# Performance work log

Hardware: AMD Instinct MI355X
Metric: run time of the kernel (lower is better)

## Reference

```python
import jax, jax.numpy as jnp
import numpy as np

N, CH = 65536, 256
B, K, CTX = 8, 256, 768
H, D = 8, 64
NPB = N // B  # points per batch (scene)


def setup_inputs() -> dict:
    key = jax.random.key(0)
    ks = jax.random.split(key, 8)
    xF = jax.random.normal(ks[0], (N, CH), dtype=jnp.float32)
    context = jax.random.normal(ks[1], (B, K, CTX), dtype=jnp.float32)
    # decomposition_permutations: a random partition of the N sparse points into B groups
    perm = jax.random.permutation(ks[2], N).reshape(B, NPB).astype(jnp.int32)
    Wq = jax.random.normal(ks[3], (CH, H * D), dtype=jnp.float32) * 0.02
    Wk = jax.random.normal(ks[4], (CTX, H * D), dtype=jnp.float32) * 0.02
    Wv = jax.random.normal(ks[5], (CTX, H * D), dtype=jnp.float32) * 0.02
    Wout = jax.random.normal(ks[6], (H * D, CH), dtype=jnp.float32) * 0.02
    b_out = jnp.zeros((CH,), dtype=jnp.float32)
    return {"xF": xF, "context": context, "perm": perm,
            "Wq": Wq, "Wk": Wk, "Wv": Wv, "Wout": Wout, "b_out": b_out}


def reference(xF, context, perm, Wq, Wk, Wv, Wout, b_out):
    scale = D ** -0.5
    q = (xF @ Wq).reshape(N, H, D)                     # to_q (1x1 conv == linear)
    k = (context @ Wk).reshape(B, K, H, D)             # to_k
    v = (context @ Wv).reshape(B, K, H, D)             # to_v
    qg = q[perm]                                        # gather: [B, NPB, H, D]
    attn = jax.nn.softmax(scale * jnp.einsum('bqhd,bkhd->bhqk', qg, k), axis=-1)
    o = jnp.einsum('bhqk,bkhd->bqhd', attn, v).reshape(B * NPB, H * D)
    # inverse-permutation scatter back to sparse-tensor order: ft[inv_perm]
    ft = jnp.zeros((N, H * D), o.dtype).at[perm.reshape(-1)].set(o)
    out = ft @ Wout + b_out                             # to_out
    return out + xF                                     # residual
```

## Files before the change

kernel.cpp:

```cpp
#include <hip/hip_runtime.h>

typedef unsigned short u16;
typedef __attribute__((ext_vector_type(8))) short bf16x8;
typedef __attribute__((ext_vector_type(4))) float f32x4;
typedef __attribute__((ext_vector_type(4))) int i32x4;
typedef __attribute__((ext_vector_type(2))) int i32x2;

#define N_PTS   65536
#define CH_DIM  256
#define BATCH   8
#define KTOK    256
#define CTX_DIM 768
#define NHEAD   8
#define HD      64
#define HDIM    512
#define NPB     8192

__device__ __forceinline__ u16 f2bf(float f) {
    union { float f; unsigned u; } v; v.f = f;
    unsigned r = v.u + 0x7fffu + ((v.u >> 16) & 1u);
    return (u16)(r >> 16);
}
__device__ __forceinline__ unsigned cvtpk(float lo, float hi) {
    unsigned r;
    asm("v_cvt_pk_bf16_f32 %0, %1, %2" : "=v"(r) : "v"(lo), "v"(hi));
    return r;
}
__device__ __forceinline__ float exp2_hw(float x) {
    float r;
    asm("v_exp_f32 %0, %1" : "=v"(r) : "v"(x));
    return r;
}
__device__ __forceinline__ float max3f(float a, float b, float c) {
    float r;
    asm("v_max3_f32 %0, %1, %2, %3" : "=v"(r) : "v"(a), "v"(b), "v"(c));
    return r;
}

__device__ __forceinline__ void gll16(const void* g, void* l) {
    __builtin_amdgcn_global_load_lds(
        (const __attribute__((address_space(1))) void*)g,
        (__attribute__((address_space(3))) void*)l, 16, 0, 0);
}

__global__ void convk(const float* __restrict__ src, u16* __restrict__ dst, int n8) {
    int i = blockIdx.x * blockDim.x + threadIdx.x;
    int st = gridDim.x * blockDim.x;
    for (; i < n8; i += st) {
        const float* p = src + (size_t)i * 8;
        f32x4 a = *(const f32x4*)p;
        f32x4 b = *(const f32x4*)(p + 4);
        i32x4 o;
        o[0] = (int)cvtpk(a[0], a[1]);
        o[1] = (int)cvtpk(a[2], a[3]);
        o[2] = (int)cvtpk(b[0], b[1]);
        o[3] = (int)cvtpk(b[2], b[3]);
        *(i32x4*)&dst[(size_t)i * 8] = o;
    }
}

__global__ void tconvk(const float* __restrict__ W, u16* __restrict__ WT, int R, int C) {
    int i = blockIdx.x * blockDim.x + threadIdx.x;
    if (i >= R * C) return;
    WT[i] = f2bf(W[(size_t)(i % R) * C + i / R]);
}

__global__ void tconv3k(const float* __restrict__ Wq, const float* __restrict__ Wk,
                        const float* __restrict__ Wv,
                        u16* __restrict__ WqT, u16* __restrict__ WkvT) {
    int i = blockIdx.x * blockDim.x + threadIdx.x;
    if (i < 131072) {
        WqT[i] = f2bf(Wq[(size_t)(i % 256) * 512 + i / 256]);
    } else if (i < 524288) {
        int j = i - 131072;
        WkvT[j] = f2bf(Wk[(size_t)(j % 768) * 512 + j / 768]);
    } else if (i < 917504) {
        int j = i - 524288;
        WkvT[393216 + j] = f2bf(Wv[(size_t)(j % 768) * 512 + j / 768]);
    }
}

template <int KC, bool OUT_F32>
__global__ __launch_bounds__(256, 3) void gemm_bt(
    const u16* __restrict__ A, const u16* __restrict__ BT, void* __restrict__ Cv,
    int M, int N,
    const float* __restrict__ bias, const float* __restrict__ resid, float oscale)
{
    __shared__ __align__(16) u16 As[2][128 * 32];
    __shared__ __align__(16) u16 Bs[2][128 * 32];

    const int tid  = threadIdx.x;
    const int lane = tid & 63;
    const int w    = tid >> 6;
    const int wm   = w & 1;
    const int wn   = w >> 1;

    const int nwg = gridDim.x * gridDim.y;
    const int wg  = blockIdx.y * gridDim.x + blockIdx.x;
    const int swz = (wg & 7) * (nwg >> 3) + (wg >> 3);
    const int n0  = (swz % gridDim.x) * 128;
    const int m0  = (swz / gridDim.x) * 128;

    const int l15  = lane & 15;
    const int quad = lane >> 4;

    f32x4 acc[4][4];
#pragma unroll
    for (int i = 0; i < 4; i++)
#pragma unroll
        for (int j = 0; j < 4; j++) { acc[i][j][0]=0.f; acc[i][j][1]=0.f; acc[i][j][2]=0.f; acc[i][j][3]=0.f; }

    const int sr = tid >> 2;
    const int sc = (tid & 3) * 8;
    const u16* Abase = A  + (size_t)(m0 + sr) * KC + sc;
    const u16* Bbase = BT + (size_t)(n0 + sr) * KC + sc;
    const size_t rowStep = (size_t)64 * KC;
    const int d8 = tid * 8;

    gll16(Abase,           &As[0][d8]);
    gll16(Abase + rowStep, &As[0][d8 + 2048]);
    gll16(Bbase,           &Bs[0][d8]);
    gll16(Bbase + rowStep, &Bs[0][d8 + 2048]);
    asm volatile("s_waitcnt vmcnt(0)" ::: "memory");
    __builtin_amdgcn_s_barrier();
    __builtin_amdgcn_sched_barrier(0);

    constexpr int ntile = KC >> 5;
    int cur = 0;
    for (int t = 0; t < ntile; ++t) {
        if (t + 1 < ntile) {
            const u16* An = Abase + ((t + 1) << 5);
            const u16* Bn = Bbase + ((t + 1) << 5);
            const int nxt = cur ^ 1;
            gll16(An,           &As[nxt][d8]);
            gll16(An + rowStep, &As[nxt][d8 + 2048]);
            gll16(Bn,           &Bs[nxt][d8]);
            gll16(Bn + rowStep, &Bs[nxt][d8 + 2048]);
        }
        bf16x8 af[4], bfr[4];
#pragma unroll
        for (int rt = 0; rt < 4; rt++)
            af[rt] = *(const bf16x8*)&As[cur][(wm * 64 + rt * 16 + l15) * 32 + quad * 8];
#pragma unroll
        for (int nt = 0; nt < 4; nt++)
            bfr[nt] = *(const bf16x8*)&Bs[cur][(wn * 64 + nt * 16 + l15) * 32 + quad * 8];
#pragma unroll
        for (int rt = 0; rt < 4; rt++)
#pragma unroll
            for (int nt = 0; nt < 4; nt++)
                acc[rt][nt] = __builtin_amdgcn_mfma_f32_16x16x32_bf16(bfr[nt], af[rt], acc[rt][nt], 0, 0, 0);
        asm volatile("s_waitcnt vmcnt(0)" ::: "memory");
        __builtin_amdgcn_sched_barrier(0);
        __builtin_amdgcn_s_barrier();
        __builtin_amdgcn_sched_barrier(0);
        cur ^= 1;
    }

    if (OUT_F32) {
#pragma unroll
        for (int rt = 0; rt < 4; rt++) {
            int m = m0 + wm * 64 + rt * 16 + l15;
#pragma unroll
            for (int nt = 0; nt < 4; nt++) {
                int nb = n0 + wn * 64 + nt * 16 + quad * 4;
                f32x4 v  = acc[rt][nt];
                f32x4 bv = *(const f32x4*)&bias[nb];
                f32x4 rv = *(const f32x4*)&resid[(size_t)m * N + nb];
#pragma unroll
                for (int r = 0; r < 4; r++) v[r] += bv[r] + rv[r];
                *(f32x4*)&((float*)Cv)[(size_t)m * N + nb] = v;
            }
        }
    } else {
#pragma unroll
        for (int rt = 0; rt < 4; rt++) {
            int m = m0 + wm * 64 + rt * 16 + l15;
#pragma unroll
            for (int nt = 0; nt < 4; nt++) {
                int nb = n0 + wn * 64 + nt * 16 + quad * 4;
                union { unsigned u[2]; i32x2 q; } pk;
                pk.u[0] = cvtpk(acc[rt][nt][0] * oscale, acc[rt][nt][1] * oscale);
                pk.u[1] = cvtpk(acc[rt][nt][2] * oscale, acc[rt][nt][3] * oscale);
                *(i32x2*)&((u16*)Cv)[(size_t)m * N + nb] = pk.q;
            }
        }
    }
}

__global__ __launch_bounds__(256, 4) void gemm_kv(
    const u16* __restrict__ A, const u16* __restrict__ BT,
    u16* __restrict__ kd, u16* __restrict__ vtd)
{
    __shared__ __align__(16) u16 As[2][64 * 32];
    __shared__ __align__(16) u16 Bs[2][64 * 32];
    const int K = CTX_DIM;

    const int tid  = threadIdx.x;
    const int lane = tid & 63;
    const int w    = tid >> 6;
    const int wm   = w & 1;
    const int wn   = w >> 1;

    const int nwg = gridDim.x * gridDim.y;
    const int wg  = blockIdx.y * gridDim.x + blockIdx.x;
    const int swz = (wg & 7) * (nwg >> 3) + (wg >> 3);
    const int n0  = (swz % gridDim.x) * 64;
    const int m0  = (swz / gridDim.x) * 64;

    const int l15  = lane & 15;
    const int quad = lane >> 4;

    f32x4 acc[2][2];
#pragma unroll
    for (int i = 0; i < 2; i++)
#pragma unroll
        for (int j = 0; j < 2; j++) { acc[i][j][0]=0.f; acc[i][j][1]=0.f; acc[i][j][2]=0.f; acc[i][j][3]=0.f; }

    const int sr = tid >> 2;
    const int sc = (tid & 3) * 8;
    const u16* Abase = A  + (size_t)(m0 + sr) * K + sc;
    const u16* Bbase = BT + (size_t)(n0 + sr) * K + sc;
    const int d8 = tid * 8;

    gll16(Abase, &As[0][d8]);
    gll16(Bbase, &Bs[0][d8]);
    asm volatile("s_waitcnt vmcnt(0)" ::: "memory");
    __builtin_amdgcn_s_barrier();
    __builtin_amdgcn_sched_barrier(0);

    const int ntile = K >> 5;
    int cur = 0;
    for (int t = 0; t < ntile; ++t) {
        if (t + 1 < ntile) {
            const int nxt = cur ^ 1;
            gll16(Abase + ((t + 1) << 5), &As[nxt][d8]);
            gll16(Bbase + ((t + 1) << 5), &Bs[nxt][d8]);
        }
        bf16x8 af[2], bfr[2];
#pragma unroll
        for (int rt = 0; rt < 2; rt++)
            af[rt] = *(const bf16x8*)&As[cur][(wm * 32 + rt * 16 + l15) * 32 + quad * 8];
#pragma unroll
        for (int nt = 0; nt < 2; nt++)
            bfr[nt] = *(const bf16x8*)&Bs[cur][(wn * 32 + nt * 16 + l15) * 32 + quad * 8];
#pragma unroll
        for (int rt = 0; rt < 2; rt++)
#pragma unroll
            for (int nt = 0; nt < 2; nt++)
                acc[rt][nt] = __builtin_amdgcn_mfma_f32_16x16x32_bf16(af[rt], bfr[nt], acc[rt][nt], 0, 0, 0);
        asm volatile("s_waitcnt vmcnt(0)" ::: "memory");
        __builtin_amdgcn_sched_barrier(0);
        __builtin_amdgcn_s_barrier();
        __builtin_amdgcn_sched_barrier(0);
        cur ^= 1;
    }

    if (n0 < 512) {
#pragma unroll
        for (int nt = 0; nt < 2; nt++) {
            int col = n0 + wn * 32 + nt * 16 + l15;
#pragma unroll
            for (int rt = 0; rt < 2; rt++) {
#pragma unroll
                for (int r = 0; r < 4; r++) {
                    int row = m0 + wm * 32 + rt * 16 + quad * 4 + r;
                    kd[(size_t)row * HDIM + col] = f2bf(acc[rt][nt][r]);
                }
            }
        }
    } else {
#pragma unroll
        for (int nt = 0; nt < 2; nt++) {
            int col = (n0 - 512) + wn * 32 + nt * 16 + l15;
            int hh = col >> 6, dd = col & 63;
#pragma unroll
            for (int rt = 0; rt < 2; rt++) {
                int row = m0 + wm * 32 + rt * 16 + quad * 4;
                int bb = row >> 8, jb = row & 255;
                int jp = (jb & 0xE0) | ((jb & 0x0C) << 1) | ((jb & 0x10) >> 2);
                union { unsigned u[2]; i32x2 q; } pk;
                pk.u[0] = cvtpk(acc[rt][nt][0], acc[rt][nt][1]);
                pk.u[1] = cvtpk(acc[rt][nt][2], acc[rt][nt][3]);
                *(i32x2*)&vtd[(((size_t)(bb * 8 + hh)) * 64 + dd) * 256 + jp] = pk.q;
            }
        }
    }
}

#define KS2 72
#define VS2 264
__global__ __launch_bounds__(256, 4) void attn_mfma(
    const u16* qbuf, const u16* __restrict__ kbuf,
    const u16* __restrict__ vbufT, const int* __restrict__ perm,
    u16* ft)
{
    __shared__ __align__(16) u16 smem[18432];
    u16* Ks = smem;
    u16* Vt = smem;

    const int tid   = threadIdx.x;
    const int lane  = tid & 63;
    const int w     = tid >> 6;
    const int chunk = blockIdx.x;
    const int bh    = blockIdx.y;
    const int b     = bh >> 3;
    const int h     = bh & 7;
    const int l15   = lane & 15;
    const int quad  = lane >> 4;

    const int prow = perm[b * NPB + chunk * 64 + w * 16 + l15];
    const u16* qrow = qbuf + (size_t)prow * HDIM + h * HD;
    bf16x8 qf0 = *(const bf16x8*)&qrow[quad * 8];
    bf16x8 qf1 = *(const bf16x8*)&qrow[32 + quad * 8];

    {
        const int j8 = tid >> 3;
        const int c  = (tid & 7) * 8;
#pragma unroll
        for (int pass = 0; pass < 8; pass++) {
            int jj = j8 + pass * 32;
            i32x4 val = *(const i32x4*)&kbuf[((size_t)(b * KTOK + jj)) * HDIM + h * HD + c];
            *(i32x4*)&Ks[jj * KS2 + c] = val;
        }
    }
    __syncthreads();

    f32x4 sc[16];
#pragma unroll
    for (int nt = 0; nt < 16; nt++) { sc[nt][0]=0.f; sc[nt][1]=0.f; sc[nt][2]=0.f; sc[nt][3]=0.f; }
#pragma unroll
    for (int nt = 0; nt < 16; nt++) {
        bf16x8 kf = *(const bf16x8*)&Ks[(nt * 16 + l15) * KS2 + quad * 8];
        sc[nt] = __builtin_amdgcn_mfma_f32_16x16x32_bf16(kf, qf0, sc[nt], 0, 0, 0);
    }
#pragma unroll
    for (int nt = 0; nt < 16; nt++) {
        bf16x8 kf = *(const bf16x8*)&Ks[(nt * 16 + l15) * KS2 + 32 + quad * 8];
        sc[nt] = __builtin_amdgcn_mfma_f32_16x16x32_bf16(kf, qf1, sc[nt], 0, 0, 0);
    }

    i32x4 vreg[8];
    const u16* vslice = vbufT + ((size_t)(b * NHEAD + h)) * HD * KTOK;
    const int vrow = tid >> 2;
    const int vc0  = (tid & 3) * 8;
#pragma unroll
    for (int pass = 0; pass < 8; pass++)
        vreg[pass] = *(const i32x4*)&vslice[(size_t)vrow * KTOK + vc0 + pass * 32];

    float m = -1e30f;
#pragma unroll
    for (int nt = 0; nt < 16; nt++) {
        f32x4 v = sc[nt];
        m = max3f(m, max3f(v[0], v[1], v[2]), v[3]);
    }
    m = fmaxf(m, __shfl_xor(m, 16));
    m = fmaxf(m, __shfl_xor(m, 32));
    float s0 = 0.f, s1 = 0.f, s2 = 0.f, s3 = 0.f;
#pragma unroll
    for (int nt = 0; nt < 16; nt++) {
        float e0 = exp2_hw(sc[nt][0] - m);
        float e1 = exp2_hw(sc[nt][1] - m);
        float e2 = exp2_hw(sc[nt][2] - m);
        float e3 = exp2_hw(sc[nt][3] - m);
        sc[nt][0] = e0; sc[nt][1] = e1; sc[nt][2] = e2; sc[nt][3] = e3;
        s0 += e0; s1 += e1; s2 += e2; s3 += e3;
    }
    float s = (s0 + s1) + (s2 + s3);
    s += __shfl_xor(s, 16);
    s += __shfl_xor(s, 32);
    float inv = 1.0f / s;

    unsigned up[16][2];
#pragma unroll
    for (int nt = 0; nt < 16; nt++) {
        up[nt][0] = cvtpk(sc[nt][0], sc[nt][1]);
        up[nt][1] = cvtpk(sc[nt][2], sc[nt][3]);
    }

    __syncthreads();

#pragma unroll
    for (int pass = 0; pass < 8; pass++)
        *(i32x4*)&Vt[vrow * VS2 + vc0 + pass * 32] = vreg[pass];
    __syncthreads();

    f32x4 o[4];
#pragma unroll
    for (int n = 0; n < 4; n++) { o[n][0]=0.f; o[n][1]=0.f; o[n][2]=0.f; o[n][3]=0.f; }

#pragma unroll
    for (int ks = 0; ks < 8; ks++) {
        union { unsigned u[4]; bf16x8 v; } pb;
        pb.u[0] = up[2 * ks][0];
        pb.u[1] = up[2 * ks][1];
        pb.u[2] = up[2 * ks + 1][0];
        pb.u[3] = up[2 * ks + 1][1];
#pragma unroll
        for (int nt = 0; nt < 4; nt++) {
            bf16x8 bv = *(const bf16x8*)&Vt[(nt * 16 + l15) * VS2 + ks * 32 + quad * 8];
            o[nt] = __builtin_amdgcn_mfma_f32_16x16x32_bf16(pb.v, bv, o[nt], 0, 0, 0);
        }
    }

#pragma unroll
    for (int r = 0; r < 4; r++) {
        float invq = __shfl(inv,  quad * 4 + r);
        int   po   = __shfl(prow, quad * 4 + r);
        u16* frow = ft + (size_t)po * HDIM + h * HD;
        unsigned pa = cvtpk(o[0][r] * invq, o[1][r] * invq);
        unsigned pb = cvtpk(o[2][r] * invq, o[3][r] * invq);
        frow[l15]      = (u16)pa;
        frow[16 + l15] = (u16)(pa >> 16);
        frow[32 + l15] = (u16)pb;
        frow[48 + l15] = (u16)(pb >> 16);
    }
}

extern "C" void kernel_launch(void* const* d_in, const int* in_sizes, int n_in,
                              void* d_out, int out_size, void* d_ws, size_t ws_size,
                              hipStream_t stream) {
    const float* xF      = (const float*)d_in[0];
    const float* context = (const float*)d_in[1];
    const int*   perm    = (const int*)d_in[2];
    const float* Wq      = (const float*)d_in[3];
    const float* Wk      = (const float*)d_in[4];
    const float* Wv      = (const float*)d_in[5];
    const float* Wout    = (const float*)d_in[6];
    const float* b_out   = (const float*)d_in[7];
    float*       out     = (float*)d_out;

    const size_t WS_NEED = 71303168ULL;
    if (ws_size < WS_NEED) {
        hipMemsetAsync(d_out, 0, (size_t)out_size * sizeof(float), stream);
        return;
    }
    char* ws    = (char*)d_ws;
    u16* kbuf   = (u16*)(ws + 0);
    u16* vbufT  = (u16*)(ws + 2097152);
    u16* qbuf   = (u16*)(ws + 4194304);
    u16* ft     = qbuf;
    u16* WoutT  = (u16*)(ws + 2097152);

    char* ob    = (char*)d_out;
    u16* xb     = (u16*)(ob + 0);
    u16* cb     = (u16*)(ob + 33554432);
    u16* WkvT   = (u16*)(ob + 36700160);
    u16* WqT    = (u16*)(ob + 38273024);

    convk<<<2048, 256, 0, stream>>>(xF, xb, N_PTS * CH_DIM / 8);
    convk<<<768, 256, 0, stream>>>(context, cb, BATCH * KTOK * CTX_DIM / 8);
    tconv3k<<<3584, 256, 0, stream>>>(Wq, Wk, Wv, WqT, WkvT);

    gemm_bt<CH_DIM, false><<<dim3(HDIM / 128, N_PTS / 128), 256, 0, stream>>>(
        xb, WqT, qbuf, N_PTS, HDIM, nullptr, nullptr, 0.1803368801f);
    gemm_kv<<<dim3(16, 32), 256, 0, stream>>>(cb, WkvT, kbuf, vbufT);

    attn_mfma<<<dim3(NPB / 64, BATCH * NHEAD), 256, 0, stream>>>(
        qbuf, kbuf, vbufT, perm, ft);

    tconvk<<<(HDIM * CH_DIM + 255) / 256, 256, 0, stream>>>(Wout, WoutT, HDIM, CH_DIM);
    gemm_bt<HDIM, true><<<dim3(CH_DIM / 128, N_PTS / 128), 256, 0, stream>>>(
        ft, WoutT, out, N_PTS, CH_DIM, b_out, xF, 1.0f);
}
```

Measured before the change: 282.3 us.

## Fuse fp32-to-bf16 input conversion into GEMM loaders and vectorize attention output stores

Drops the separate convk passes over xF and context. The Q-projection and KV GEMMs now load fp32 A tiles into registers, pack them to bf16 and write them to LDS themselves. The attention PV MFMA operands are swapped so each lane holds a contiguous run of output columns for its own row, letting the scatter to ft use 8-byte stores instead of shuffles and 2-byte stores. The cost is that A loads now go through registers instead of direct global-to-LDS loads, which adds register pressure and LDS write latency inside the pipelined loop.

```diff
diff --git a/kernel.cpp b/kernel.cpp
--- a/kernel.cpp
+++ b/kernel.cpp
@@ -43,20 +43,13 @@
         (__attribute__((address_space(3))) void*)l, 16, 0, 0);
 }
 
-__global__ void convk(const float* __restrict__ src, u16* __restrict__ dst, int n8) {
-    int i = blockIdx.x * blockDim.x + threadIdx.x;
-    int st = gridDim.x * blockDim.x;
-    for (; i < n8; i += st) {
-        const float* p = src + (size_t)i * 8;
-        f32x4 a = *(const f32x4*)p;
-        f32x4 b = *(const f32x4*)(p + 4);
-        i32x4 o;
-        o[0] = (int)cvtpk(a[0], a[1]);
-        o[1] = (int)cvtpk(a[2], a[3]);
-        o[2] = (int)cvtpk(b[0], b[1]);
-        o[3] = (int)cvtpk(b[2], b[3]);
-        *(i32x4*)&dst[(size_t)i * 8] = o;
-    }
+__device__ __forceinline__ i32x4 pk8(f32x4 a, f32x4 b) {
+    i32x4 o;
+    o[0] = (int)cvtpk(a[0], a[1]);
+    o[1] = (int)cvtpk(a[2], a[3]);
+    o[2] = (int)cvtpk(b[0], b[1]);
+    o[3] = (int)cvtpk(b[2], b[3]);
+    return o;
 }
 
 __global__ void tconvk(const float* __restrict__ W, u16* __restrict__ WT, int R, int C) {
@@ -80,9 +73,9 @@
     }
 }
 
-template <int KC, bool OUT_F32>
+template <int KC, bool A_F32, bool OUT_F32>
 __global__ __launch_bounds__(256, 3) void gemm_bt(
-    const u16* __restrict__ A, const u16* __restrict__ BT, void* __restrict__ Cv,
+    const void* __restrict__ Av, const u16* __restrict__ BT, void* __restrict__ Cv,
     int M, int N,
     const float* __restrict__ bias, const float* __restrict__ resid, float oscale)
 {
@@ -112,28 +105,53 @@
 
     const int sr = tid >> 2;
     const int sc = (tid & 3) * 8;
-    const u16* Abase = A  + (size_t)(m0 + sr) * KC + sc;
+    const u16*   Ab = (const u16*)Av;
+    const float* Af = (const float*)Av;
+    const u16* Abase = Ab + (size_t)(m0 + sr) * KC + sc;
+    const float* Fbase = Af + (size_t)(m0 + sr) * KC + sc;
     const u16* Bbase = BT + (size_t)(n0 + sr) * KC + sc;
     const size_t rowStep = (size_t)64 * KC;
     const int d8 = tid * 8;
 
-    gll16(Abase,           &As[0][d8]);
-    gll16(Abase + rowStep, &As[0][d8 + 2048]);
+    f32x4 a0, a1, a2, a3;
+
+    if (A_F32) {
+        a0 = *(const f32x4*)&Fbase[0];
+        a1 = *(const f32x4*)&Fbase[4];
+        a2 = *(const f32x4*)&Fbase[rowStep];
+        a3 = *(const f32x4*)&Fbase[rowStep + 4];
+    } else {
+        gll16(Abase,           &As[0][d8]);
+        gll16(Abase + rowStep, &As[0][d8 + 2048]);
+    }
     gll16(Bbase,           &Bs[0][d8]);
     gll16(Bbase + rowStep, &Bs[0][d8 + 2048]);
     asm volatile("s_waitcnt vmcnt(0)" ::: "memory");
+    if (A_F32) {
+        *(i32x4*)&As[0][d8]        = pk8(a0, a1);
+        *(i32x4*)&As[0][d8 + 2048] = pk8(a2, a3);
+    }
+    asm volatile("s_waitcnt lgkmcnt(0)" ::: "memory");
     __builtin_amdgcn_s_barrier();
     __builtin_amdgcn_sched_barrier(0);
 
     constexpr int ntile = KC >> 5;
     int cur = 0;
     for (int t = 0; t < ntile; ++t) {
+        const int nxt = cur ^ 1;
         if (t + 1 < ntile) {
-            const u16* An = Abase + ((t + 1) << 5);
+            if (A_F32) {
+                const float* Fn = Fbase + (size_t)((t + 1) << 5);
+                a0 = *(const f32x4*)&Fn[0];
+                a1 = *(const f32x4*)&Fn[4];
+                a2 = *(const f32x4*)&Fn[rowStep];
+                a3 = *(const f32x4*)&Fn[rowStep + 4];
+            } else {
+                const u16* An = Abase + ((t + 1) << 5);
+                gll16(An,           &As[nxt][d8]);
+                gll16(An + rowStep, &As[nxt][d8 + 2048]);
+            }
             const u16* Bn = Bbase + ((t + 1) << 5);
-            const int nxt = cur ^ 1;
-            gll16(An,           &As[nxt][d8]);
-            gll16(An + rowStep, &As[nxt][d8 + 2048]);
             gll16(Bn,           &Bs[nxt][d8]);
             gll16(Bn + rowStep, &Bs[nxt][d8 + 2048]);
         }
@@ -150,6 +168,11 @@
             for (int nt = 0; nt < 4; nt++)
                 acc[rt][nt] = __builtin_amdgcn_mfma_f32_16x16x32_bf16(bfr[nt], af[rt], acc[rt][nt], 0, 0, 0);
         asm volatile("s_waitcnt vmcnt(0)" ::: "memory");
+        if (A_F32 && t + 1 < ntile) {
+            *(i32x4*)&As[nxt][d8]        = pk8(a0, a1);
+            *(i32x4*)&As[nxt][d8 + 2048] = pk8(a2, a3);
+        }
+        asm volatile("s_waitcnt lgkmcnt(0)" ::: "memory");
         __builtin_amdgcn_sched_barrier(0);
         __builtin_amdgcn_s_barrier();
         __builtin_amdgcn_sched_barrier(0);
@@ -188,7 +211,7 @@
 }
 
 __global__ __launch_bounds__(256, 4) void gemm_kv(
-    const u16* __restrict__ A, const u16* __restrict__ BT,
+    const float* __restrict__ A, const u16* __restrict__ BT,
     u16* __restrict__ kd, u16* __restrict__ vtd)
 {
     __shared__ __align__(16) u16 As[2][64 * 32];
@@ -218,22 +241,28 @@
 
     const int sr = tid >> 2;
     const int sc = (tid & 3) * 8;
-    const u16* Abase = A  + (size_t)(m0 + sr) * K + sc;
-    const u16* Bbase = BT + (size_t)(n0 + sr) * K + sc;
+    const float* Fbase = A + (size_t)(m0 + sr) * K + sc;
+    const u16*   Bbase = BT + (size_t)(n0 + sr) * K + sc;
     const int d8 = tid * 8;
 
-    gll16(Abase, &As[0][d8]);
+    f32x4 a0, a1;
+    a0 = *(const f32x4*)&Fbase[0];
+    a1 = *(const f32x4*)&Fbase[4];
     gll16(Bbase, &Bs[0][d8]);
     asm volatile("s_waitcnt vmcnt(0)" ::: "memory");
+    *(i32x4*)&As[0][d8] = pk8(a0, a1);
+    asm volatile("s_waitcnt lgkmcnt(0)" ::: "memory");
     __builtin_amdgcn_s_barrier();
     __builtin_amdgcn_sched_barrier(0);
 
     const int ntile = K >> 5;
     int cur = 0;
     for (int t = 0; t < ntile; ++t) {
+        const int nxt = cur ^ 1;
         if (t + 1 < ntile) {
-            const int nxt = cur ^ 1;
-            gll16(Abase + ((t + 1) << 5), &As[nxt][d8]);
+            const float* Fn = Fbase + ((t + 1) << 5);
+            a0 = *(const f32x4*)&Fn[0];
+            a1 = *(const f32x4*)&Fn[4];
             gll16(Bbase + ((t + 1) << 5), &Bs[nxt][d8]);
         }
         bf16x8 af[2], bfr[2];
@@ -249,6 +278,9 @@
             for (int nt = 0; nt < 2; nt++)
                 acc[rt][nt] = __builtin_amdgcn_mfma_f32_16x16x32_bf16(af[rt], bfr[nt], acc[rt][nt], 0, 0, 0);
         asm volatile("s_waitcnt vmcnt(0)" ::: "memory");
+        if (t + 1 < ntile)
+            *(i32x4*)&As[nxt][d8] = pk8(a0, a1);
+        asm volatile("s_waitcnt lgkmcnt(0)" ::: "memory");
         __builtin_amdgcn_sched_barrier(0);
         __builtin_amdgcn_s_barrier();
         __builtin_amdgcn_sched_barrier(0);
@@ -397,22 +429,20 @@
         pb.u[3] = up[2 * ks + 1][1];
 #pragma unroll
         for (int nt = 0; nt < 4; nt++) {
-            bf16x8 bv = *(const bf16x8*)&Vt[(nt * 16 + l15) * VS2 + ks * 32 + quad * 8];
-            o[nt] = __builtin_amdgcn_mfma_f32_16x16x32_bf16(pb.v, bv, o[nt], 0, 0, 0);
-        }
-    }
-
-#pragma unroll
-    for (int r = 0; r < 4; r++) {
-        float invq = __shfl(inv,  quad * 4 + r);
-        int   po   = __shfl(prow, quad * 4 + r);
-        u16* frow = ft + (size_t)po * HDIM + h * HD;
-        unsigned pa = cvtpk(o[0][r] * invq, o[1][r] * invq);
-        unsigned pb = cvtpk(o[2][r] * invq, o[3][r] * invq);
-        frow[l15]      = (u16)pa;
-        frow[16 + l15] = (u16)(pa >> 16);
-        frow[32 + l15] = (u16)pb;
-        frow[48 + l15] = (u16)(pb >> 16);
+            bf16x8 av = *(const bf16x8*)&Vt[(nt * 16 + l15) * VS2 + ks * 32 + quad * 8];
+            o[nt] = __builtin_amdgcn_mfma_f32_16x16x32_bf16(av, pb.v, o[nt], 0, 0, 0);
+        }
+    }
+
+    {
+        u16* frow = ft + (size_t)prow * HDIM + h * HD;
+#pragma unroll
+        for (int nt = 0; nt < 4; nt++) {
+            union { unsigned u[2]; i32x2 q; } pk;
+            pk.u[0] = cvtpk(o[nt][0] * inv, o[nt][1] * inv);
+            pk.u[1] = cvtpk(o[nt][2] * inv, o[nt][3] * inv);
+            *(i32x2*)&frow[nt * 16 + quad * 4] = pk.q;
+        }
     }
 }
 
@@ -442,23 +472,19 @@
     u16* WoutT  = (u16*)(ws + 2097152);
 
     char* ob    = (char*)d_out;
-    u16* xb     = (u16*)(ob + 0);
-    u16* cb     = (u16*)(ob + 33554432);
-    u16* WkvT   = (u16*)(ob + 36700160);
-    u16* WqT    = (u16*)(ob + 38273024);
-
-    convk<<<2048, 256, 0, stream>>>(xF, xb, N_PTS * CH_DIM / 8);
-    convk<<<768, 256, 0, stream>>>(context, cb, BATCH * KTOK * CTX_DIM / 8);
+    u16* WkvT   = (u16*)(ob + 0);
+    u16* WqT    = (u16*)(ob + 1572864);
+
     tconv3k<<<3584, 256, 0, stream>>>(Wq, Wk, Wv, WqT, WkvT);
 
-    gemm_bt<CH_DIM, false><<<dim3(HDIM / 128, N_PTS / 128), 256, 0, stream>>>(
-        xb, WqT, qbuf, N_PTS, HDIM, nullptr, nullptr, 0.1803368801f);
-    gemm_kv<<<dim3(16, 32), 256, 0, stream>>>(cb, WkvT, kbuf, vbufT);
+    gemm_bt<CH_DIM, true, false><<<dim3(HDIM / 128, N_PTS / 128), 256, 0, stream>>>(
+        xF, WqT, qbuf, N_PTS, HDIM, nullptr, nullptr, 0.1803368801f);
+    gemm_kv<<<dim3(16, 32), 256, 0, stream>>>(context, WkvT, kbuf, vbufT);
 
     attn_mfma<<<dim3(NPB / 64, BATCH * NHEAD), 256, 0, stream>>>(
         qbuf, kbuf, vbufT, perm, ft);
 
     tconvk<<<(HDIM * CH_DIM + 255) / 256, 256, 0, stream>>>(Wout, WoutT, HDIM, CH_DIM);
-    gemm_bt<HDIM, true><<<dim3(CH_DIM / 128, N_PTS / 128), 256, 0, stream>>>(
+    gemm_bt<HDIM, false, true><<<dim3(CH_DIM / 128, N_PTS / 128), 256, 0, stream>>>(
         ft, WoutT, out, N_PTS, CH_DIM, b_out, xF, 1.0f);
 }
```

Result: slower. 306.7 us (+8.6%).

## Process two query tiles per attention block to reuse staged K/V

Applied to the files above, without the earlier changes.

Each attention block now handles 128 query rows instead of 64, computing scores and softmax for two 16-row tiles per wave against the same K and V tiles held in shared memory. The grid is halved, so each K/V load into shared memory is amortised over twice the queries. The PV MFMA operands are swapped so that the output comes out transposed, which allows packed 8-byte stores of four bf16 values per lane into ft instead of scalar u16 stores. The cost is higher register pressure (two sets of packed probabilities and accumulators) and fewer blocks to fill the machine.

```diff
diff --git a/kernel.cpp b/kernel.cpp
--- a/kernel.cpp
+++ b/kernel.cpp
@@ -307,11 +307,12 @@
     const int h     = bh & 7;
     const int l15   = lane & 15;
     const int quad  = lane >> 4;
-
-    const int prow = perm[b * NPB + chunk * 64 + w * 16 + l15];
-    const u16* qrow = qbuf + (size_t)prow * HDIM + h * HD;
-    bf16x8 qf0 = *(const bf16x8*)&qrow[quad * 8];
-    bf16x8 qf1 = *(const bf16x8*)&qrow[32 + quad * 8];
+    const int qbase = b * NPB + chunk * 128;
+
+    const int prowA = perm[qbase + w * 16 + l15];
+    const u16* qrowA = qbuf + (size_t)prowA * HDIM + h * HD;
+    bf16x8 qA0 = *(const bf16x8*)&qrowA[quad * 8];
+    bf16x8 qA1 = *(const bf16x8*)&qrowA[32 + quad * 8];
 
     {
         const int j8 = tid >> 3;
@@ -326,17 +327,64 @@
     __syncthreads();
 
     f32x4 sc[16];
+    unsigned upA[16][2], upB[16][2];
+    float invA, invB;
+
 #pragma unroll
     for (int nt = 0; nt < 16; nt++) { sc[nt][0]=0.f; sc[nt][1]=0.f; sc[nt][2]=0.f; sc[nt][3]=0.f; }
 #pragma unroll
     for (int nt = 0; nt < 16; nt++) {
         bf16x8 kf = *(const bf16x8*)&Ks[(nt * 16 + l15) * KS2 + quad * 8];
-        sc[nt] = __builtin_amdgcn_mfma_f32_16x16x32_bf16(kf, qf0, sc[nt], 0, 0, 0);
+        sc[nt] = __builtin_amdgcn_mfma_f32_16x16x32_bf16(kf, qA0, sc[nt], 0, 0, 0);
     }
 #pragma unroll
     for (int nt = 0; nt < 16; nt++) {
         bf16x8 kf = *(const bf16x8*)&Ks[(nt * 16 + l15) * KS2 + 32 + quad * 8];
-        sc[nt] = __builtin_amdgcn_mfma_f32_16x16x32_bf16(kf, qf1, sc[nt], 0, 0, 0);
+        sc[nt] = __builtin_amdgcn_mfma_f32_16x16x32_bf16(kf, qA1, sc[nt], 0, 0, 0);
+    }
+    {
+        float m = -1e30f;
+#pragma unroll
+        for (int nt = 0; nt < 16; nt++) {
+            f32x4 v = sc[nt];
+            m = max3f(m, max3f(v[0], v[1], v[2]), v[3]);
+        }
+        m = fmaxf(m, __shfl_xor(m, 16));
+        m = fmaxf(m, __shfl_xor(m, 32));
+        float s0 = 0.f, s1 = 0.f, s2 = 0.f, s3 = 0.f;
+#pragma unroll
+        for (int nt = 0; nt < 16; nt++) {
+            float e0 = exp2_hw(sc[nt][0] - m);
+            float e1 = exp2_hw(sc[nt][1] - m);
+            float e2 = exp2_hw(sc[nt][2] - m);
+            float e3 = exp2_hw(sc[nt][3] - m);
+            upA[nt][0] = cvtpk(e0, e1);
+            upA[nt][1] = cvtpk(e2, e3);
+            s0 += e0; s1 += e1; s2 += e2; s3 += e3;
+        }
+        float s = (s0 + s1) + (s2 + s3);
+        s += __shfl_xor(s, 16);
+        s += __shfl_xor(s, 32);
+        invA = 1.0f / s;
+    }
+
+    const int prowB = perm[qbase + 64 + w * 16 + l15];
+    {
+        const u16* qrowB = qbuf + (size_t)prowB * HDIM + h * HD;
+        bf16x8 qB0 = *(const bf16x8*)&qrowB[quad * 8];
+        bf16x8 qB1 = *(const bf16x8*)&qrowB[32 + quad * 8];
+#pragma unroll
+        for (int nt = 0; nt < 16; nt++) { sc[nt][0]=0.f; sc[nt][1]=0.f; sc[nt][2]=0.f; sc[nt][3]=0.f; }
+#pragma unroll
+        for (int nt = 0; nt < 16; nt++) {
+            bf16x8 kf = *(const bf16x8*)&Ks[(nt * 16 + l15) * KS2 + quad * 8];
+            sc[nt] = __builtin_amdgcn_mfma_f32_16x16x32_bf16(kf, qB0, sc[nt], 0, 0, 0);
+        }
+#pragma unroll
+        for (int nt = 0; nt < 16; nt++) {
+            bf16x8 kf = *(const bf16x8*)&Ks[(nt * 16 + l15) * KS2 + 32 + quad * 8];
+            sc[nt] = __builtin_amdgcn_mfma_f32_16x16x32_bf16(kf, qB1, sc[nt], 0, 0, 0);
+        }
     }
 
     i32x4 vreg[8];
@@ -347,34 +395,30 @@
     for (int pass = 0; pass < 8; pass++)
         vreg[pass] = *(const i32x4*)&vslice[(size_t)vrow * KTOK + vc0 + pass * 32];
 
-    float m = -1e30f;
-#pragma unroll
-    for (int nt = 0; nt < 16; nt++) {
-        f32x4 v = sc[nt];
-        m = max3f(m, max3f(v[0], v[1], v[2]), v[3]);
-    }
-    m = fmaxf(m, __shfl_xor(m, 16));
-    m = fmaxf(m, __shfl_xor(m, 32));
-    float s0 = 0.f, s1 = 0.f, s2 = 0.f, s3 = 0.f;
-#pragma unroll
-    for (int nt = 0; nt < 16; nt++) {
-        float e0 = exp2_hw(sc[nt][0] - m);
-        float e1 = exp2_hw(sc[nt][1] - m);
-        float e2 = exp2_hw(sc[nt][2] - m);
-        float e3 = exp2_hw(sc[nt][3] - m);
-        sc[nt][0] = e0; sc[nt][1] = e1; sc[nt][2] = e2; sc[nt][3] = e3;
-        s0 += e0; s1 += e1; s2 += e2; s3 += e3;
-    }
-    float s = (s0 + s1) + (s2 + s3);
-    s += __shfl_xor(s, 16);
-    s += __shfl_xor(s, 32);
-    float inv = 1.0f / s;
-
-    unsigned up[16][2];
-#pragma unroll
-    for (int nt = 0; nt < 16; nt++) {
-        up[nt][0] = cvtpk(sc[nt][0], sc[nt][1]);
-        up[nt][1] = cvtpk(sc[nt][2], sc[nt][3]);
+    {
+        float m = -1e30f;
+#pragma unroll
+        for (int nt = 0; nt < 16; nt++) {
+            f32x4 v = sc[nt];
+            m = max3f(m, max3f(v[0], v[1], v[2]), v[3]);
+        }
+        m = fmaxf(m, __shfl_xor(m, 16));
+        m = fmaxf(m, __shfl_xor(m, 32));
+        float s0 = 0.f, s1 = 0.f, s2 = 0.f, s3 = 0.f;
+#pragma unroll
+        for (int nt = 0; nt < 16; nt++) {
+            float e0 = exp2_hw(sc[nt][0] - m);
+            float e1 = exp2_hw(sc[nt][1] - m);
+            float e2 = exp2_hw(sc[nt][2] - m);
+            float e3 = exp2_hw(sc[nt][3] - m);
+            upB[nt][0] = cvtpk(e0, e1);
+            upB[nt][1] = cvtpk(e2, e3);
+            s0 += e0; s1 += e1; s2 += e2; s3 += e3;
+        }
+        float s = (s0 + s1) + (s2 + s3);
+        s += __shfl_xor(s, 16);
+        s += __shfl_xor(s, 32);
+        invB = 1.0f / s;
     }
 
     __syncthreads();
@@ -384,35 +428,48 @@
         *(i32x4*)&Vt[vrow * VS2 + vc0 + pass * 32] = vreg[pass];
     __syncthreads();
 
-    f32x4 o[4];
-#pragma unroll
-    for (int n = 0; n < 4; n++) { o[n][0]=0.f; o[n][1]=0.f; o[n][2]=0.f; o[n][3]=0.f; }
-
+    f32x4 oA[4], oB[4];
+#pragma unroll
+    for (int n = 0; n < 4; n++) {
+        oA[n][0]=0.f; oA[n][1]=0.f; oA[n][2]=0.f; oA[n][3]=0.f;
+        oB[n][0]=0.f; oB[n][1]=0.f; oB[n][2]=0.f; oB[n][3]=0.f;
+    }
 #pragma unroll
     for (int ks = 0; ks < 8; ks++) {
-        union { unsigned u[4]; bf16x8 v; } pb;
-        pb.u[0] = up[2 * ks][0];
-        pb.u[1] = up[2 * ks][1];
-        pb.u[2] = up[2 * ks + 1][0];
-        pb.u[3] = up[2 * ks + 1][1];
+        union { unsigned u[4]; bf16x8 v; } pa, pb;
+        pa.u[0] = upA[2 * ks][0];
+        pa.u[1] = upA[2 * ks][1];
+        pa.u[2] = upA[2 * ks + 1][0];
+        pa.u[3] = upA[2 * ks + 1][1];
+        pb.u[0] = upB[2 * ks][0];
+        pb.u[1] = upB[2 * ks][1];
+        pb.u[2] = upB[2 * ks + 1][0];
+        pb.u[3] = upB[2 * ks + 1][1];
 #pragma unroll
         for (int nt = 0; nt < 4; nt++) {
-            bf16x8 bv = *(const bf16x8*)&Vt[(nt * 16 + l15) * VS2 + ks * 32 + quad * 8];
-            o[nt] = __builtin_amdgcn_mfma_f32_16x16x32_bf16(pb.v, bv, o[nt], 0, 0, 0);
-        }
-    }
-
-#pragma unroll
-    for (int r = 0; r < 4; r++) {
-        float invq = __shfl(inv,  quad * 4 + r);
-        int   po   = __shfl(prow, quad * 4 + r);
-        u16* frow = ft + (size_t)po * HDIM + h * HD;
-        unsigned pa = cvtpk(o[0][r] * invq, o[1][r] * invq);
-        unsigned pb = cvtpk(o[2][r] * invq, o[3][r] * invq);
-        frow[l15]      = (u16)pa;
-        frow[16 + l15] = (u16)(pa >> 16);
-        frow[32 + l15] = (u16)pb;
-        frow[48 + l15] = (u16)(pb >> 16);
+            bf16x8 av = *(const bf16x8*)&Vt[(nt * 16 + l15) * VS2 + ks * 32 + quad * 8];
+            oA[nt] = __builtin_amdgcn_mfma_f32_16x16x32_bf16(av, pa.v, oA[nt], 0, 0, 0);
+            oB[nt] = __builtin_amdgcn_mfma_f32_16x16x32_bf16(av, pb.v, oB[nt], 0, 0, 0);
+        }
+    }
+
+    {
+        u16* frowA = ft + (size_t)prowA * HDIM + h * HD;
+#pragma unroll
+        for (int nt = 0; nt < 4; nt++) {
+            union { unsigned u[2]; i32x2 q; } pk;
+            pk.u[0] = cvtpk(oA[nt][0] * invA, oA[nt][1] * invA);
+            pk.u[1] = cvtpk(oA[nt][2] * invA, oA[nt][3] * invA);
+            *(i32x2*)&frowA[nt * 16 + quad * 4] = pk.q;
+        }
+        u16* frowB = ft + (size_t)prowB * HDIM + h * HD;
+#pragma unroll
+        for (int nt = 0; nt < 4; nt++) {
+            union { unsigned u[2]; i32x2 q; } pk;
+            pk.u[0] = cvtpk(oB[nt][0] * invB, oB[nt][1] * invB);
+            pk.u[1] = cvtpk(oB[nt][2] * invB, oB[nt][3] * invB);
+            *(i32x2*)&frowB[nt * 16 + quad * 4] = pk.q;
+        }
     }
 }
 
@@ -455,7 +512,7 @@
         xb, WqT, qbuf, N_PTS, HDIM, nullptr, nullptr, 0.1803368801f);
     gemm_kv<<<dim3(16, 32), 256, 0, stream>>>(cb, WkvT, kbuf, vbufT);
 
-    attn_mfma<<<dim3(NPB / 64, BATCH * NHEAD), 256, 0, stream>>>(
+    attn_mfma<<<dim3(NPB / 128, BATCH * NHEAD), 256, 0, stream>>>(
         qbuf, kbuf, vbufT, perm, ft);
 
     tconvk<<<(HDIM * CH_DIM + 255) / 256, 256, 0, stream>>>(Wout, WoutT, HDIM, CH_DIM);
```

Result: slower. 602.9 us (+113.5%).
